# Kernel optimization log

Hardware: AMD Instinct MI355X
Metric: run time of the kernel (lower is better)

The kernel has to match this reference:

```python
import jax, jax.numpy as jnp
import numpy as np

HIDDEN = 2048
INTER = 768
N_EXPERTS = 8
TOP_K = 2
BATCH, SEQ = 4, 512


def setup_inputs() -> dict:
    key = jax.random.key(0)
    ks = jax.random.split(key, 5)
    std = 0.02
    hidden_states = jax.random.normal(ks[0], (BATCH, SEQ, HIDDEN), dtype=jnp.float32)
    W_gate = jax.random.normal(ks[1], (N_EXPERTS, HIDDEN), dtype=jnp.float32) * std  # router Linear weight [E,H]
    Wg = jax.random.normal(ks[2], (N_EXPERTS, HIDDEN, INTER), dtype=jnp.float32) * std  # gate proj per expert
    Wu = jax.random.normal(ks[3], (N_EXPERTS, HIDDEN, INTER), dtype=jnp.float32) * std  # up proj per expert
    Wd = jax.random.normal(ks[4], (N_EXPERTS, INTER, HIDDEN), dtype=jnp.float32) * std  # down proj per expert
    return {"hidden_states": hidden_states, "W_gate": W_gate, "Wg": Wg, "Wu": Wu, "Wd": Wd}


def reference(hidden_states, W_gate, Wg, Wu, Wd):
    orig_shape = hidden_states.shape
    x = hidden_states.reshape(-1, HIDDEN)              # [T, H]
    T = x.shape[0]

    # Router: softmax in float32, top-k, renormalize (matches torch code).
    router_logits = x @ W_gate.T                        # [T, E]
    routing_probs = jax.nn.softmax(router_logits.astype(jnp.float32), axis=-1)
    topk_w, topk_idx = jax.lax.top_k(routing_probs, TOP_K)  # [T, K]
    topk_w = topk_w / jnp.sum(topk_w, axis=-1, keepdims=True)
    topk_w = topk_w.astype(x.dtype)

    # Sparse combine weights as dense [T, E] (equiv to index_add over torch.where dispatch).
    combine = jnp.zeros((T, N_EXPERTS), dtype=x.dtype)
    combine = combine.at[jnp.arange(T)[:, None], topk_idx].add(topk_w)

    # Expert MLPs, computed densely over experts (idiomatic jit-able dispatch).
    g = jnp.einsum('th,ehi->eti', x, Wg)                # [E, T, I]
    u = jnp.einsum('th,ehi->eti', x, Wu)                # [E, T, I]
    h = jax.nn.silu(g) * u                              # SiluAndMul
    y = jnp.einsum('eti,eih->eth', h, Wd)               # [E, T, H]

    out = jnp.einsum('eth,te->th', y, combine)          # weighted combine
    return out.reshape(orig_shape)
```

## Files before the change

kernel.cpp:

```cpp
#include <hip/hip_runtime.h>
#include <hip/hip_bf16.h>
#include <math.h>

#define H_DIM 2048
#define I_DIM 768
#define NEXP  8
#define TTOK  2048

typedef __bf16 bf16x8 __attribute__((ext_vector_type(8)));
typedef __bf16 bf16x4 __attribute__((ext_vector_type(4)));
typedef float  f32x4  __attribute__((ext_vector_type(4)));

#define WS_COUNTS   0u
#define WS_TOK      128u
#define WS_WGTW     65664u
#define WS_XBF      131328u
#define WS_HBUF     8519936u
#define WS_WG_T     15008000u
#define WS_WU_T     40173824u
#define WS_WD_T     65339648u

__device__ __forceinline__ void gl2l(const __bf16* g, __bf16* l) {
    __builtin_amdgcn_global_load_lds(
        (const __attribute__((address_space(1))) unsigned int*)g,
        (__attribute__((address_space(3))) unsigned int*)l, 16, 0, 0);
}

__device__ __forceinline__ void pipe_sync_vm8() {
    asm volatile("" ::: "memory");
    __builtin_amdgcn_s_waitcnt(0x78);
    __builtin_amdgcn_s_barrier();
    asm volatile("" ::: "memory");
}
__device__ __forceinline__ void pipe_sync_vm4() {
    asm volatile("" ::: "memory");
    __builtin_amdgcn_s_waitcnt(0x74);
    __builtin_amdgcn_s_barrier();
    asm volatile("" ::: "memory");
}
__device__ __forceinline__ void pipe_sync_vm0() {
    asm volatile("" ::: "memory");
    __builtin_amdgcn_s_waitcnt(0x70);
    __builtin_amdgcn_s_barrier();
    asm volatile("" ::: "memory");
}

#define NTRANS 18432
__global__ __launch_bounds__(128) void prep_k(
    const float* __restrict__ x, const float* __restrict__ Wgate,
    const float* __restrict__ Wg, const float* __restrict__ Wu, const float* __restrict__ Wd,
    int* __restrict__ counts, int* __restrict__ tok_list, float* __restrict__ wgt,
    __bf16* __restrict__ xb, __bf16* __restrict__ Wg_t, __bf16* __restrict__ Wu_t,
    __bf16* __restrict__ Wd_t) {
    __shared__ float sT[64 * 33];
    __shared__ float s_red[NEXP][2];
    __shared__ float s_logit[NEXP];
    const int tid = threadIdx.x;
    const int b = blockIdx.x;

    if (b >= NTRANS) {
        const int t = b - NTRANS;
        const float4* xr = (const float4*)(x + (size_t)t * H_DIM);
        bf16x4* xo = (bf16x4*)(xb + (size_t)t * H_DIM);
        float acc[NEXP];
#pragma unroll
        for (int e = 0; e < NEXP; ++e) acc[e] = 0.f;
#pragma unroll
        for (int j = 0; j < 4; ++j) {
            const int i4 = j * 128 + tid;
            float4 v = xr[i4];
            bf16x4 o;
            o[0] = (__bf16)v.x; o[1] = (__bf16)v.y; o[2] = (__bf16)v.z; o[3] = (__bf16)v.w;
            xo[i4] = o;
#pragma unroll
            for (int e = 0; e < NEXP; ++e) {
                float4 wv = *(const float4*)(Wgate + e * H_DIM + i4 * 4);
                acc[e] += v.x * wv.x + v.y * wv.y + v.z * wv.z + v.w * wv.w;
            }
        }
        const int lane = tid & 63, w = tid >> 6;
#pragma unroll
        for (int e = 0; e < NEXP; ++e) {
            float v = acc[e];
#pragma unroll
            for (int off = 32; off > 0; off >>= 1) v += __shfl_down(v, off, 64);
            if (lane == 0) s_red[e][w] = v;
        }
        __syncthreads();
        if (tid < NEXP) s_logit[tid] = s_red[tid][0] + s_red[tid][1];
        __syncthreads();
        if (tid == 0) {
            int i0 = 0; float l0 = s_logit[0];
            for (int e = 1; e < NEXP; ++e) if (s_logit[e] > l0) { l0 = s_logit[e]; i0 = e; }
            int i1 = -1; float l1 = -1e30f;
            for (int e = 0; e < NEXP; ++e) if (e != i0 && s_logit[e] > l1) { l1 = s_logit[e]; i1 = e; }
            float w0 = 1.f / (1.f + expf(l1 - l0));
            float w1 = 1.f - w0;
            int p0 = atomicAdd(&counts[i0], 1);
            tok_list[i0 * TTOK + p0] = t; wgt[i0 * TTOK + p0] = w0;
            int p1 = atomicAdd(&counts[i1], 1);
            tok_list[i1 * TTOK + p1] = t; wgt[i1 * TTOK + p1] = w1;
        }
        return;
    }

    int r = b;
    const int t3 = r / 6144; r -= t3 * 6144;
    const int e = r / 768;  const int rem = r - e * 768;
    const float* in; __bf16* out; int K, N, k0, n0;
    if (t3 < 2) { K = H_DIM; N = I_DIM; k0 = (rem / 12) * 32; n0 = (rem % 12) * 64;
                  in = t3 ? Wu : Wg; out = t3 ? Wu_t : Wg_t; }
    else        { K = I_DIM; N = H_DIM; k0 = (rem / 32) * 32; n0 = (rem % 32) * 64;
                  in = Wd; out = Wd_t; }
    const float* ip = in + (size_t)e * K * N;
    const int kl = tid >> 4;
    const int n4 = (tid & 15) * 4;
#pragma unroll
    for (int j = 0; j < 4; ++j) {
        int k = kl + j * 8;
        float4 v = *(const float4*)(ip + (size_t)(k0 + k) * N + n0 + n4);
        sT[(n4 + 0) * 33 + k] = v.x;
        sT[(n4 + 1) * 33 + k] = v.y;
        sT[(n4 + 2) * 33 + k] = v.z;
        sT[(n4 + 3) * 33 + k] = v.w;
    }
    __syncthreads();
    const int n = tid >> 1;
    const int kc = (tid & 1) * 16;
    bf16x8 o0, o1;
#pragma unroll
    for (int j = 0; j < 8; ++j) {
        o0[j] = (__bf16)sT[n * 33 + kc + j];
        o1[j] = (__bf16)sT[n * 33 + kc + 8 + j];
    }
    __bf16* op = out + (size_t)e * N * K + (size_t)(n0 + n) * K + k0 + kc;
    *(bf16x8*)op = o0;
    *(bf16x8*)(op + 8) = o1;
}

__global__ __launch_bounds__(256, 2) void gemm1_k(
    const __bf16* __restrict__ xb, const __bf16* __restrict__ Wgt,
    const __bf16* __restrict__ Wut, const int* __restrict__ counts,
    const int* __restrict__ tok_list, __bf16* __restrict__ hbuf) {
    const int lin = blockIdx.x;
    const int xcd = lin & 7, t6 = lin >> 3;
    const int sG = t6 / 12, nt = t6 % 12;
    const int G = (sG << 3) | xcd;
    const int e = G >> 4, y = G & 15;
    const int cnt = counts[e];
    const int m0 = y * 128;
    if (m0 >= cnt) return;
    const int tid = threadIdx.x;
    const int lane = tid & 63, w = tid >> 6;

    __shared__ __bf16 sA[4][128 * 32];
    __shared__ __bf16 sG_[4][64 * 32];
    __shared__ __bf16 sU[4][64 * 32];
    __shared__ int s_tok[128];
    __shared__ int s_off;

    if (tid == 0) { int o = 0; for (int j = 0; j < e; ++j) o += counts[j]; s_off = o; }
    if (tid < 128) {
        int m = m0 + tid;
        s_tok[tid] = tok_list[e * TTOK + (m < cnt ? m : cnt - 1)];
    }
    __syncthreads();
    const int off = s_off;

    const int srow = lane >> 2;
    const int gof = ((lane & 3) ^ (srow & 3)) * 8;
    const __bf16* pA[2]; int lofA[2];
#pragma unroll
    for (int i = 0; i < 2; ++i) {
        int r = i * 64 + w * 16 + srow;
        pA[i] = xb + (size_t)s_tok[r] * H_DIM + gof;
        lofA[i] = (i * 64 + w * 16) * 32;
    }
    const __bf16 *pG, *pU;
    const int lofGU = (w * 16) * 32;
    {
        int r = w * 16 + srow;
        size_t grow = (size_t)e * I_DIM + nt * 64 + r;
        pG = Wgt + grow * H_DIM + gof;
        pU = Wut + grow * H_DIM + gof;
    }

    const int wm = w & 1, wn = w >> 1;
    const int l15 = lane & 15, kq = lane >> 4;
    const int swz = (kq ^ (l15 & 3)) * 8;

    f32x4 accG[4][2], accU[4][2];
#pragma unroll
    for (int mf = 0; mf < 4; ++mf)
#pragma unroll
        for (int nf = 0; nf < 2; ++nf) {
            accG[mf][nf] = (f32x4){0.f, 0.f, 0.f, 0.f};
            accU[mf][nf] = (f32x4){0.f, 0.f, 0.f, 0.f};
        }

#define G1_ISSUE(T, BUF)                                             \
    {                                                                \
        const int kb_ = (T) * 32;                                    \
        gl2l(pA[0] + kb_, &sA[BUF][lofA[0]]);                        \
        gl2l(pA[1] + kb_, &sA[BUF][lofA[1]]);                        \
        gl2l(pG + kb_, &sG_[BUF][lofGU]);                            \
        gl2l(pU + kb_, &sU[BUF][lofGU]);                             \
    }

#define G1_COMPUTE(P)                                                                    \
    {                                                                                    \
        bf16x8 af[4], bg[2], bu[2];                                                      \
        _Pragma("unroll")                                                                \
        for (int mf = 0; mf < 4; ++mf)                                                   \
            af[mf] = *(const bf16x8*)(&sA[P][0] + (wm * 64 + mf * 16 + l15) * 32 + swz); \
        _Pragma("unroll")                                                                \
        for (int nf = 0; nf < 2; ++nf) {                                                 \
            bg[nf] = *(const bf16x8*)(&sG_[P][0] + (wn * 32 + nf * 16 + l15) * 32 + swz);\
            bu[nf] = *(const bf16x8*)(&sU[P][0] + (wn * 32 + nf * 16 + l15) * 32 + swz); \
        }                                                                                \
        _Pragma("unroll")                                                                \
        for (int mf = 0; mf < 4; ++mf)                                                   \
            _Pragma("unroll")                                                            \
            for (int nf = 0; nf < 2; ++nf) {                                             \
                accG[mf][nf] = __builtin_amdgcn_mfma_f32_16x16x32_bf16(af[mf], bg[nf], accG[mf][nf], 0, 0, 0); \
                accU[mf][nf] = __builtin_amdgcn_mfma_f32_16x16x32_bf16(af[mf], bu[nf], accU[mf][nf], 0, 0, 0); \
            }                                                                            \
    }

    G1_ISSUE(0, 0); G1_ISSUE(1, 1); G1_ISSUE(2, 2);

#pragma unroll 4
    for (int it = 0; it < 60; ++it) {
        const int p = it & 3;
        pipe_sync_vm8();
        G1_ISSUE(it + 3, (it + 3) & 3);
        G1_COMPUTE(p);
    }
    pipe_sync_vm8(); G1_ISSUE(63, 3); G1_COMPUTE(0);
    pipe_sync_vm8(); G1_COMPUTE(1);
    pipe_sync_vm4(); G1_COMPUTE(2);
    pipe_sync_vm0(); G1_COMPUTE(3);
#undef G1_ISSUE
#undef G1_COMPUTE

#pragma unroll
    for (int mf = 0; mf < 4; ++mf) {
#pragma unroll
        for (int reg = 0; reg < 4; ++reg) {
            int m = m0 + wm * 64 + mf * 16 + kq * 4 + reg;
            if (m < cnt) {
                size_t rowbase = (size_t)(off + m) * I_DIM;
#pragma unroll
                for (int nf = 0; nf < 2; ++nf) {
                    float g1 = accG[mf][nf][reg], u1 = accU[mf][nf][reg];
                    float h = (g1 / (1.f + __expf(-g1))) * u1;
                    hbuf[rowbase + nt * 64 + wn * 32 + nf * 16 + l15] = (__bf16)h;
                }
            }
        }
    }
}

__global__ __launch_bounds__(256, 2) void gemm2_k(
    const __bf16* __restrict__ hbuf, const __bf16* __restrict__ Wdt,
    const int* __restrict__ counts, const int* __restrict__ tok_list,
    const float* __restrict__ wgt, float* __restrict__ out) {
    const int lin = blockIdx.x;
    const int xcd = lin & 7, t6 = lin >> 3;
    const int sG = t6 >> 4, nt = t6 & 15;
    const int G = (sG << 3) | xcd;
    const int e = G >> 4, y = G & 15;
    const int cnt = counts[e];
    const int m0 = y * 128;
    if (m0 >= cnt) return;
    const int tid = threadIdx.x;
    const int lane = tid & 63, w = tid >> 6;

    __shared__ __bf16 sA[4][128 * 32];
    __shared__ __bf16 sB[4][128 * 32];
    __shared__ int s_tok[128];
    __shared__ float s_w[128];
    __shared__ int s_off;

    if (tid == 0) { int o = 0; for (int j = 0; j < e; ++j) o += counts[j]; s_off = o; }
    if (tid < 128) {
        int m = m0 + tid;
        if (m < cnt) { s_tok[tid] = tok_list[e * TTOK + m]; s_w[tid] = wgt[e * TTOK + m]; }
        else         { s_tok[tid] = 0;                      s_w[tid] = 0.f; }
    }
    __syncthreads();
    const int off = s_off;

    const int srow = lane >> 2;
    const int gof = ((lane & 3) ^ (srow & 3)) * 8;
    const __bf16* pA[2]; int lofA[2];
    const __bf16* pB[2]; int lofB[2];
#pragma unroll
    for (int i = 0; i < 2; ++i) {
        int r = i * 64 + w * 16 + srow;
        pA[i] = hbuf + (size_t)(off + m0 + r) * I_DIM + gof;
        pB[i] = Wdt + ((size_t)e * H_DIM + nt * 128 + r) * I_DIM + gof;
        lofA[i] = (i * 64 + w * 16) * 32;
        lofB[i] = (i * 64 + w * 16) * 32;
    }

    const int wm = w & 1, wn = w >> 1;
    const int l15 = lane & 15, kq = lane >> 4;
    const int swz = (kq ^ (l15 & 3)) * 8;

    f32x4 acc[4][4];
#pragma unroll
    for (int mf = 0; mf < 4; ++mf)
#pragma unroll
        for (int nf = 0; nf < 4; ++nf) acc[mf][nf] = (f32x4){0.f, 0.f, 0.f, 0.f};

#define G2_ISSUE(T, BUF)                                             \
    {                                                                \
        const int kb_ = (T) * 32;                                    \
        gl2l(pA[0] + kb_, &sA[BUF][lofA[0]]);                        \
        gl2l(pA[1] + kb_, &sA[BUF][lofA[1]]);                        \
        gl2l(pB[0] + kb_, &sB[BUF][lofB[0]]);                        \
        gl2l(pB[1] + kb_, &sB[BUF][lofB[1]]);                        \
    }

#define G2_COMPUTE(P)                                                                    \
    {                                                                                    \
        bf16x8 af[4], bb[4];                                                             \
        _Pragma("unroll")                                                                \
        for (int mf = 0; mf < 4; ++mf)                                                   \
            af[mf] = *(const bf16x8*)(&sA[P][0] + (wm * 64 + mf * 16 + l15) * 32 + swz); \
        _Pragma("unroll")                                                                \
        for (int nf = 0; nf < 4; ++nf)                                                   \
            bb[nf] = *(const bf16x8*)(&sB[P][0] + (wn * 64 + nf * 16 + l15) * 32 + swz); \
        _Pragma("unroll")                                                                \
        for (int mf = 0; mf < 4; ++mf)                                                   \
            _Pragma("unroll")                                                            \
            for (int nf = 0; nf < 4; ++nf)                                               \
                acc[mf][nf] = __builtin_amdgcn_mfma_f32_16x16x32_bf16(af[mf], bb[nf], acc[mf][nf], 0, 0, 0); \
    }

    G2_ISSUE(0, 0); G2_ISSUE(1, 1); G2_ISSUE(2, 2);
#pragma unroll 4
    for (int it = 0; it < 20; ++it) {
        const int p = it & 3;
        pipe_sync_vm8();
        G2_ISSUE(it + 3, (it + 3) & 3);
        G2_COMPUTE(p);
    }
    pipe_sync_vm8(); G2_ISSUE(23, 3); G2_COMPUTE(0);
    pipe_sync_vm8(); G2_COMPUTE(1);
    pipe_sync_vm4(); G2_COMPUTE(2);
    pipe_sync_vm0(); G2_COMPUTE(3);
#undef G2_ISSUE
#undef G2_COMPUTE

#pragma unroll
    for (int mf = 0; mf < 4; ++mf) {
#pragma unroll
        for (int reg = 0; reg < 4; ++reg) {
            int m_loc = wm * 64 + mf * 16 + kq * 4 + reg;
            if (m0 + m_loc < cnt) {
                int tok = s_tok[m_loc];
                float wv = s_w[m_loc];
                float* orow = out + (size_t)tok * H_DIM + nt * 128 + wn * 64 + l15;
#pragma unroll
                for (int nf = 0; nf < 4; ++nf)
                    atomicAdd(orow + nf * 16, wv * acc[mf][nf][reg]);
            }
        }
    }
}

extern "C" void kernel_launch(void* const* d_in, const int* in_sizes, int n_in,
                              void* d_out, int out_size, void* d_ws, size_t ws_size,
                              hipStream_t stream) {
    const float* x     = (const float*)d_in[0];
    const float* Wgate = (const float*)d_in[1];
    const float* Wg    = (const float*)d_in[2];
    const float* Wu    = (const float*)d_in[3];
    const float* Wd    = (const float*)d_in[4];
    float* out = (float*)d_out;
    char* ws = (char*)d_ws;

    int*    counts   = (int*)(ws + WS_COUNTS);
    int*    tok_list = (int*)(ws + WS_TOK);
    float*  wgt      = (float*)(ws + WS_WGTW);
    __bf16* xb       = (__bf16*)(ws + WS_XBF);
    __bf16* hbuf     = (__bf16*)(ws + WS_HBUF);
    __bf16* Wg_t     = (__bf16*)(ws + WS_WG_T);
    __bf16* Wu_t     = (__bf16*)(ws + WS_WU_T);
    __bf16* Wd_t     = (__bf16*)(ws + WS_WD_T);

    hipMemsetAsync(counts, 0, 32, stream);
    hipMemsetAsync(d_out, 0, (size_t)TTOK * H_DIM * sizeof(float), stream);

    prep_k<<<NTRANS + TTOK, 128, 0, stream>>>(x, Wgate, Wg, Wu, Wd,
                                              counts, tok_list, wgt, xb, Wg_t, Wu_t, Wd_t);
    gemm1_k<<<96 * 16, 256, 0, stream>>>(xb, Wg_t, Wu_t, counts, tok_list, hbuf);
    gemm2_k<<<128 * 16, 256, 0, stream>>>(hbuf, Wd_t, counts, tok_list, wgt, out);
}
```

Baseline: 396.4 us.

## Store transposed expert weights in pre-tiled swizzled blocks and drop XCD grid remap

```diff
diff --git a/kernel.cpp b/kernel.cpp
--- a/kernel.cpp
+++ b/kernel.cpp
@@ -19,6 +19,7 @@
 #define WS_WG_T     15008000u
 #define WS_WU_T     40173824u
 #define WS_WD_T     65339648u
+
 
 __device__ __forceinline__ void gl2l(const __bf16* g, __bf16* l) {
     __builtin_amdgcn_global_load_lds(
@@ -107,12 +108,24 @@
     int r = b;
     const int t3 = r / 6144; r -= t3 * 6144;
     const int e = r / 768;  const int rem = r - e * 768;
-    const float* in; __bf16* out; int K, N, k0, n0;
-    if (t3 < 2) { K = H_DIM; N = I_DIM; k0 = (rem / 12) * 32; n0 = (rem % 12) * 64;
-                  in = t3 ? Wu : Wg; out = t3 ? Wu_t : Wg_t; }
-    else        { K = I_DIM; N = H_DIM; k0 = (rem / 32) * 32; n0 = (rem % 32) * 64;
-                  in = Wd; out = Wd_t; }
-    const float* ip = in + (size_t)e * K * N;
+    const float* in; __bf16* out; int N, k0, n0;
+    size_t tbase; int rowbase;
+    if (t3 < 2) {
+        N = I_DIM;
+        const int kt = rem / 12, nt = rem % 12;
+        k0 = kt * 32; n0 = nt * 64;
+        in = t3 ? Wu : Wg; out = t3 ? Wu_t : Wg_t;
+        tbase = ((size_t)(e * 12 + nt) * 64 + kt) * 2048;
+        rowbase = 0;
+    } else {
+        N = H_DIM;
+        const int kt = rem / 32, ntraw = rem % 32;
+        k0 = kt * 32; n0 = ntraw * 64;
+        in = Wd; out = Wd_t;
+        tbase = ((size_t)(e * 16 + (ntraw >> 1)) * 24 + kt) * 4096;
+        rowbase = (ntraw & 1) * 64;
+    }
+    const float* ip = in + (size_t)e * (N == I_DIM ? H_DIM * I_DIM : I_DIM * H_DIM);
     const int kl = tid >> 4;
     const int n4 = (tid & 15) * 4;
 #pragma unroll
@@ -125,30 +138,28 @@
         sT[(n4 + 3) * 33 + k] = v.w;
     }
     __syncthreads();
-    const int n = tid >> 1;
-    const int kc = (tid & 1) * 16;
+    const int rn = tid >> 1;
+    const int c0 = (tid & 1) * 2;
     bf16x8 o0, o1;
 #pragma unroll
     for (int j = 0; j < 8; ++j) {
-        o0[j] = (__bf16)sT[n * 33 + kc + j];
-        o1[j] = (__bf16)sT[n * 33 + kc + 8 + j];
-    }
-    __bf16* op = out + (size_t)e * N * K + (size_t)(n0 + n) * K + k0 + kc;
-    *(bf16x8*)op = o0;
-    *(bf16x8*)(op + 8) = o1;
+        o0[j] = (__bf16)sT[rn * 33 + c0 * 8 + j];
+        o1[j] = (__bf16)sT[rn * 33 + c0 * 8 + 8 + j];
+    }
+    const int s0 = c0 ^ (rn & 3), s1 = s0 ^ 1;
+    __bf16* op = out + tbase + (size_t)(rowbase + rn) * 32;
+    *(bf16x8*)(op + s0 * 8) = o0;
+    *(bf16x8*)(op + s1 * 8) = o1;
 }
 
 __global__ __launch_bounds__(256, 2) void gemm1_k(
     const __bf16* __restrict__ xb, const __bf16* __restrict__ Wgt,
     const __bf16* __restrict__ Wut, const int* __restrict__ counts,
     const int* __restrict__ tok_list, __bf16* __restrict__ hbuf) {
-    const int lin = blockIdx.x;
-    const int xcd = lin & 7, t6 = lin >> 3;
-    const int sG = t6 / 12, nt = t6 % 12;
-    const int G = (sG << 3) | xcd;
-    const int e = G >> 4, y = G & 15;
+    const int g = blockIdx.x;
+    const int e = g / 12, nt = g % 12;
     const int cnt = counts[e];
-    const int m0 = y * 128;
+    const int m0 = blockIdx.y * 128;
     if (m0 >= cnt) return;
     const int tid = threadIdx.x;
     const int lane = tid & 63, w = tid >> 6;
@@ -176,14 +187,9 @@
         pA[i] = xb + (size_t)s_tok[r] * H_DIM + gof;
         lofA[i] = (i * 64 + w * 16) * 32;
     }
-    const __bf16 *pG, *pU;
     const int lofGU = (w * 16) * 32;
-    {
-        int r = w * 16 + srow;
-        size_t grow = (size_t)e * I_DIM + nt * 64 + r;
-        pG = Wgt + grow * H_DIM + gof;
-        pU = Wut + grow * H_DIM + gof;
-    }
+    const __bf16* pG = Wgt + (size_t)(e * 12 + nt) * 64 * 2048 + w * 512 + lane * 8;
+    const __bf16* pU = Wut + (size_t)(e * 12 + nt) * 64 * 2048 + w * 512 + lane * 8;
 
     const int wm = w & 1, wn = w >> 1;
     const int l15 = lane & 15, kq = lane >> 4;
@@ -200,11 +206,10 @@
 
 #define G1_ISSUE(T, BUF)                                             \
     {                                                                \
-        const int kb_ = (T) * 32;                                    \
-        gl2l(pA[0] + kb_, &sA[BUF][lofA[0]]);                        \
-        gl2l(pA[1] + kb_, &sA[BUF][lofA[1]]);                        \
-        gl2l(pG + kb_, &sG_[BUF][lofGU]);                            \
-        gl2l(pU + kb_, &sU[BUF][lofGU]);                             \
+        gl2l(pA[0] + (T) * 32, &sA[BUF][lofA[0]]);                   \
+        gl2l(pA[1] + (T) * 32, &sA[BUF][lofA[1]]);                   \
+        gl2l(pG + (T) * 2048, &sG_[BUF][lofGU]);                     \
+        gl2l(pU + (T) * 2048, &sU[BUF][lofGU]);                      \
     }
 
 #define G1_COMPUTE(P)                                                                    \
@@ -265,13 +270,10 @@
     const __bf16* __restrict__ hbuf, const __bf16* __restrict__ Wdt,
     const int* __restrict__ counts, const int* __restrict__ tok_list,
     const float* __restrict__ wgt, float* __restrict__ out) {
-    const int lin = blockIdx.x;
-    const int xcd = lin & 7, t6 = lin >> 3;
-    const int sG = t6 >> 4, nt = t6 & 15;
-    const int G = (sG << 3) | xcd;
-    const int e = G >> 4, y = G & 15;
+    const int g = blockIdx.x;
+    const int e = g >> 4, nt = g & 15;
     const int cnt = counts[e];
-    const int m0 = y * 128;
+    const int m0 = blockIdx.y * 128;
     if (m0 >= cnt) return;
     const int tid = threadIdx.x;
     const int lane = tid & 63, w = tid >> 6;
@@ -294,15 +296,16 @@
     const int srow = lane >> 2;
     const int gof = ((lane & 3) ^ (srow & 3)) * 8;
     const __bf16* pA[2]; int lofA[2];
-    const __bf16* pB[2]; int lofB[2];
 #pragma unroll
     for (int i = 0; i < 2; ++i) {
         int r = i * 64 + w * 16 + srow;
         pA[i] = hbuf + (size_t)(off + m0 + r) * I_DIM + gof;
-        pB[i] = Wdt + ((size_t)e * H_DIM + nt * 128 + r) * I_DIM + gof;
         lofA[i] = (i * 64 + w * 16) * 32;
-        lofB[i] = (i * 64 + w * 16) * 32;
-    }
+    }
+    const int lofB0 = (w * 16) * 32;
+    const int lofB1 = (64 + w * 16) * 32;
+    const __bf16* pB0 = Wdt + (size_t)(e * 16 + nt) * 24 * 4096 + (w * 16) * 32 + lane * 8;
+    const __bf16* pB1 = pB0 + 64 * 32;
 
     const int wm = w & 1, wn = w >> 1;
     const int l15 = lane & 15, kq = lane >> 4;
@@ -316,11 +319,10 @@
 
 #define G2_ISSUE(T, BUF)                                             \
     {                                                                \
-        const int kb_ = (T) * 32;                                    \
-        gl2l(pA[0] + kb_, &sA[BUF][lofA[0]]);                        \
-        gl2l(pA[1] + kb_, &sA[BUF][lofA[1]]);                        \
-        gl2l(pB[0] + kb_, &sB[BUF][lofB[0]]);                        \
-        gl2l(pB[1] + kb_, &sB[BUF][lofB[1]]);                        \
+        gl2l(pA[0] + (T) * 32, &sA[BUF][lofA[0]]);                   \
+        gl2l(pA[1] + (T) * 32, &sA[BUF][lofA[1]]);                   \
+        gl2l(pB0 + (T) * 4096, &sB[BUF][lofB0]);                     \
+        gl2l(pB1 + (T) * 4096, &sB[BUF][lofB1]);                     \
     }
 
 #define G2_COMPUTE(P)                                                                    \
@@ -396,6 +398,6 @@
 
     prep_k<<<NTRANS + TTOK, 128, 0, stream>>>(x, Wgate, Wg, Wu, Wd,
                                               counts, tok_list, wgt, xb, Wg_t, Wu_t, Wd_t);
-    gemm1_k<<<96 * 16, 256, 0, stream>>>(xb, Wg_t, Wu_t, counts, tok_list, hbuf);
-    gemm2_k<<<128 * 16, 256, 0, stream>>>(hbuf, Wd_t, counts, tok_list, wgt, out);
-}
+    gemm1_k<<<dim3(96, 16), 256, 0, stream>>>(xb, Wg_t, Wu_t, counts, tok_list, hbuf);
+    gemm2_k<<<dim3(128, 16), 256, 0, stream>>>(hbuf, Wd_t, counts, tok_list, wgt, out);
+}
```

Result: faster. 340.4 us (-14.1%).
